# Kernel optimization log

Measured on AMD Instinct MI355X. Metric: run time of the kernel, lower is better.

The kernel has to match this reference:

```python
import jax, jax.numpy as jnp
import numpy as np

B, S, IN, OUT, H, L, NH, STEPS = 256, 128, 64, 64, 1024, 2, 4, 16
HD = H // NH


def setup_inputs() -> dict:
    key = jax.random.key(0)
    ks = iter(jax.random.split(key, 32))
    std_h = 1.0 / np.sqrt(H)

    def u(k, shape, std):
        return jax.random.uniform(k, shape, jnp.float32, -std, std)

    inp = {"x": jax.random.normal(next(ks), (B, S, IN), jnp.float32)}
    # LSTM cells: stacked gate weights, gate order (i, f, g, o); y = x@Wx + h@Wh + b
    for name, din in (("e0", IN), ("e1", H), ("d0", OUT), ("d1", H)):
        inp[name + "_Wx"] = u(next(ks), (din, 4 * H), std_h)
        inp[name + "_Wh"] = u(next(ks), (H, 4 * H), std_h)
        inp[name + "_b"] = u(next(ks), (4 * H,), std_h)
    # attention linears (x@W + b convention)
    for name in ("Wq", "Wk", "Wv", "Wo"):
        inp[name] = u(next(ks), (H, H), std_h)
    for name in ("bq", "bk", "bv", "bo"):
        inp[name] = u(next(ks), (H,), std_h)
    inp["fc_W"] = u(next(ks), (2 * H, H), 1.0 / np.sqrt(2 * H))
    inp["fc_b"] = u(next(ks), (H,), 1.0 / np.sqrt(2 * H))
    inp["out_W"] = u(next(ks), (H, OUT), std_h)
    inp["out_b"] = u(next(ks), (OUT,), std_h)
    return inp


def _cell(x_t, h, c, Wx, Wh, b):
    z = x_t @ Wx + h @ Wh + b  # [B, 4H]
    i, f, g, o = jnp.split(z, 4, axis=-1)
    c = jax.nn.sigmoid(f) * c + jax.nn.sigmoid(i) * jnp.tanh(g)
    h = jax.nn.sigmoid(o) * jnp.tanh(c)
    return h, c


def _lstm_seq(x, Wx, Wh, b):
    # x: [B, T, D] -> outputs [B, T, H], final (h, c)
    h0 = jnp.zeros((x.shape[0], H), x.dtype)
    def step(carry, xt):
        h, c = carry
        h, c = _cell(xt, h, c, Wx, Wh, b)
        return (h, c), h
    (h, c), ys = jax.lax.scan(step, (h0, h0), jnp.swapaxes(x, 0, 1))
    return jnp.swapaxes(ys, 0, 1), h, c


def reference(x, e0_Wx, e0_Wh, e0_b, e1_Wx, e1_Wh, e1_b,
              d0_Wx, d0_Wh, d0_b, d1_Wx, d1_Wh, d1_b,
              Wq, bq, Wk, bk, Wv, bv, Wo, bo, fc_W, fc_b, out_W, out_b):
    # encoder: 2-layer manual LSTM (dropout=0, eval)
    y0, h0, c0 = _lstm_seq(x, e0_Wx, e0_Wh, e0_b)
    enc_out, h1, c1 = _lstm_seq(y0, e1_Wx, e1_Wh, e1_b)

    # K/V projections of encoder outputs (constant across decoder steps)
    Kp = (enc_out @ Wk + bk).reshape(B, S, NH, HD)
    Vp = (enc_out @ Wv + bv).reshape(B, S, NH, HD)
    scale = float(HD) ** 0.5

    def dstep(carry, _):
        dh0, dc0, dh1, dc1, xin = carry
        dh0, dc0 = _cell(xin, dh0, dc0, d0_Wx, d0_Wh, d0_b)
        dh1, dc1 = _cell(dh0, dh1, dc1, d1_Wx, d1_Wh, d1_b)
        q = (dh1 @ Wq + bq).reshape(B, NH, HD)
        scores = jnp.einsum('bnd,bsnd->bns', q, Kp) / scale
        w = jax.nn.softmax(scores, axis=-1)
        ctx = jnp.einsum('bns,bsnd->bnd', w, Vp).reshape(B, H)
        attn = ctx @ Wo + bo
        comb = jax.nn.relu(jnp.concatenate([dh1, attn], axis=-1) @ fc_W + fc_b)
        out = comb @ out_W + out_b  # [B, OUT]
        return (dh0, dc0, dh1, dc1, out), out

    init = (h0, c0, h1, c1, jnp.zeros((B, OUT), x.dtype))
    _, preds = jax.lax.scan(dstep, init, None, length=STEPS)
    return jnp.swapaxes(preds, 0, 1)  # [B, STEPS, OUT]
```

## Files before the change

kernel.cpp:

```cpp
#include <hip/hip_runtime.h>
#include <math.h>

typedef _Float16 h8 __attribute__((ext_vector_type(8)));
typedef _Float16 h4 __attribute__((ext_vector_type(4)));
typedef float f16v __attribute__((ext_vector_type(16)));

#define HPS 262144
#define XPS 2097152
#define IPS 16384
#define BSTR 40
#define BUFE (128 * BSTR)

__device__ __forceinline__ float4 ld4(const float* p) { return *(const float4*)p; }
__device__ __forceinline__ float sigf(float x) { return 1.0f / (1.0f + expf(-x)); }
__device__ __forceinline__ float bf2f(unsigned short u) { return __uint_as_float(((unsigned)u) << 16); }
__device__ __forceinline__ float rdin(const void* p, size_t i, int bf) {
  return bf ? bf2f(((const unsigned short*)p)[i]) : ((const float*)p)[i];
}

__global__ void detect_dtype(const unsigned short* __restrict__ probe, int n, int* flag) {
  __shared__ int cnt;
  if (threadIdx.x == 0) cnt = 0;
  __syncthreads();
  int c = 0;
  for (int i = threadIdx.x; i < n; i += 256) {
    int e = (probe[i] >> 7) & 0xFF;
    if (e >= 100 && e <= 126) c++;
  }
  atomicAdd(&cnt, c);
  __syncthreads();
  if (threadIdx.x == 0) *flag = (cnt > (n * 3) / 4) ? 1 : 0;
}

__global__ void cvt_f32(const void* __restrict__ in, float* __restrict__ out, int n,
                        const int* __restrict__ flag) {
  int bf = *flag;
  int i = blockIdx.x * 256 + threadIdx.x;
  if (i < n) out[i] = rdin(in, i, bf);
}

__global__ void tsplit(const void* __restrict__ in, int N,
                       _Float16* __restrict__ outHi, _Float16* __restrict__ outLo,
                       int ldo, int kOff, int pOff, const int* __restrict__ flag) {
  __shared__ float tile[32][33];
  int bf = *flag;
  int kb = blockIdx.x * 32, nb = blockIdx.y * 32;
  for (int r = threadIdx.y; r < 32; r += 8)
    tile[threadIdx.x][r] = rdin(in, (size_t)(kb + r) * N + nb + threadIdx.x, bf);
  __syncthreads();
  for (int r = threadIdx.y; r < 32; r += 8) {
    float v = tile[r][threadIdx.x];
    _Float16 hi = (_Float16)v;
    _Float16 lo = (_Float16)(v - (float)hi);
    size_t o = (size_t)(pOff + nb + r) * ldo + kOff + kb + threadIdx.x;
    outHi[o] = hi; outLo[o] = lo;
  }
}

__global__ void f2h_kernel(const void* __restrict__ in, _Float16* __restrict__ out, int n,
                           const int* __restrict__ flag) {
  int bf = *flag;
  int i = blockIdx.x * 1024 + threadIdx.x * 4;
  if (i < n) {
    float vv[4];
#pragma unroll
    for (int k = 0; k < 4; ++k) vv[k] = rdin(in, i + k, bf);
    h4 hv, lv;
#pragma unroll
    for (int k = 0; k < 4; ++k) { hv[k] = (_Float16)vv[k]; lv[k] = (_Float16)(vv[k] - (float)hv[k]); }
    *(h4*)(out + i) = hv;
    *(h4*)(out + n + i) = lv;
  }
}

__global__ void sentinel_kernel(float* out, float v) { out[0] = v; }

__device__ __forceinline__ void gemm_tile(
    const _Float16* __restrict__ A0, int lda0, int aps0,
    const _Float16* __restrict__ A1, int lda1, int aps1, int ksplit,
    const _Float16* __restrict__ WTh, const _Float16* __restrict__ WTl, int ldw,
    int pbase, int c0, int c1,
    float* __restrict__ zp, int zld, _Float16* Bs ) {
  const int tid = threadIdx.x;
  const int wv = tid >> 6, lane = tid & 63;
  const int l31 = lane & 31, lhi = lane >> 5;

  f16v acc00 = {}, acc01 = {}, acc10 = {}, acc11 = {};

  const int r0 = wv * 64 + l31;
  const int r1 = r0 + 32;
  const _Float16* a0b0 = A0 + (size_t)r0 * lda0;
  const _Float16* a1b0 = A1 + (size_t)r0 * lda1;
  const _Float16* a0b1 = A0 + (size_t)r1 * lda0;
  const _Float16* a1b1 = A1 + (size_t)r1 * lda1;

  const int spl = tid >> 7;
  const int sidx = tid & 127;
  const int sp = sidx >> 1;
  const int skh = (sidx & 1) << 4;
  const _Float16* srow = (spl ? WTl : WTh) + (size_t)(pbase + sp) * ldw + skh;
  const int sdoff = (spl * 64 + sp) * BSTR + skh;

  {
    const _Float16* s = srow + (c0 << 5);
    float4 v0 = *(const float4*)(s);
    float4 v1 = *(const float4*)(s + 8);
    _Float16* d = Bs + sdoff;
    *(float4*)(d) = v0;
    *(float4*)(d + 8) = v1;
  }

  int buf = 0;
  for (int c = c0; c < c1; ++c) {
    __syncthreads();
    float4 n0, n1;
    const bool more = (c + 1 < c1);
    if (more) {
      const _Float16* s = srow + ((c + 1) << 5);
      n0 = *(const float4*)(s);
      n1 = *(const float4*)(s + 8);
    }
    const _Float16* bb = Bs + buf * BUFE;
    int k0 = c << 5;
#pragma unroll
    for (int sub = 0; sub < 2; ++sub) {
      int ks = k0 + sub * 16 + lhi * 8;
      const _Float16 *pa0, *pa1; int ap;
      if (ks < ksplit) { pa0 = a0b0 + ks; pa1 = a0b1 + ks; ap = aps0; }
      else { int kk = ks - ksplit; pa0 = a1b0 + kk; pa1 = a1b1 + kk; ap = aps1; }
      h8 af0h = *(const h8*)pa0;
      h8 af0l = *(const h8*)(pa0 + ap);
      h8 af1h = *(const h8*)pa1;
      h8 af1l = *(const h8*)(pa1 + ap);
      int kl = sub * 16 + lhi * 8;
      h8 b0h = *(const h8*)(bb + (size_t)(l31) * BSTR + kl);
      h8 b0l = *(const h8*)(bb + (size_t)(64 + l31) * BSTR + kl);
      h8 b1h = *(const h8*)(bb + (size_t)(32 + l31) * BSTR + kl);
      h8 b1l = *(const h8*)(bb + (size_t)(96 + l31) * BSTR + kl);
      acc00 = __builtin_amdgcn_mfma_f32_32x32x16_f16(af0h, b0h, acc00, 0, 0, 0);
      acc00 = __builtin_amdgcn_mfma_f32_32x32x16_f16(af0h, b0l, acc00, 0, 0, 0);
      acc00 = __builtin_amdgcn_mfma_f32_32x32x16_f16(af0l, b0h, acc00, 0, 0, 0);
      acc01 = __builtin_amdgcn_mfma_f32_32x32x16_f16(af0h, b1h, acc01, 0, 0, 0);
      acc01 = __builtin_amdgcn_mfma_f32_32x32x16_f16(af0h, b1l, acc01, 0, 0, 0);
      acc01 = __builtin_amdgcn_mfma_f32_32x32x16_f16(af0l, b1h, acc01, 0, 0, 0);
      acc10 = __builtin_amdgcn_mfma_f32_32x32x16_f16(af1h, b0h, acc10, 0, 0, 0);
      acc10 = __builtin_amdgcn_mfma_f32_32x32x16_f16(af1h, b0l, acc10, 0, 0, 0);
      acc10 = __builtin_amdgcn_mfma_f32_32x32x16_f16(af1l, b0h, acc10, 0, 0, 0);
      acc11 = __builtin_amdgcn_mfma_f32_32x32x16_f16(af1h, b1h, acc11, 0, 0, 0);
      acc11 = __builtin_amdgcn_mfma_f32_32x32x16_f16(af1h, b1l, acc11, 0, 0, 0);
      acc11 = __builtin_amdgcn_mfma_f32_32x32x16_f16(af1l, b1h, acc11, 0, 0, 0);
    }
    if (more) {
      _Float16* d = Bs + (buf ^ 1) * BUFE + sdoff;
      *(float4*)(d) = n0;
      *(float4*)(d + 8) = n1;
    }
    buf ^= 1;
  }

#pragma unroll
  for (int mi = 0; mi < 2; ++mi) {
#pragma unroll
    for (int ni = 0; ni < 2; ++ni) {
      f16v av = (mi == 0) ? (ni == 0 ? acc00 : acc01) : (ni == 0 ? acc10 : acc11);
      int col = pbase + ni * 32 + l31;
#pragma unroll
      for (int r = 0; r < 16; ++r) {
        int row = wv * 64 + mi * 32 + (r & 3) + ((r >> 2) * 8) + lhi * 4;
        zp[(size_t)row * zld + col] = av[r];
      }
    }
  }
}

__global__ __launch_bounds__(256, 2) void enc_gemm(int t, int l1kq,
    const _Float16* xh, const _Float16* h0, const _Float16* h1,
    const _Float16* wt0h, const _Float16* wt0l,
    const _Float16* wt1h, const _Float16* wt1l,
    const _Float16* wtkvh, const _Float16* wtkvl,
    float* z0, float* z1, float* kvz) {
  __shared__ _Float16 Bs[2 * BUFE];
  int blk = blockIdx.x;
  int nl1 = 64 * l1kq;
  if (blk < nl1) {
    if (t < 1 || t > 128) return;
    int pg = blk & 63, kq = blk >> 6;
    int c0 = (64 * kq) / l1kq, c1 = (64 * (kq + 1)) / l1kq;
    gemm_tile(h0, 1024, HPS, h1, 1024, HPS, 1024, wt1h, wt1l, 2048,
              pg * 64, c0, c1, z1 + (size_t)kq * 1048576, 4096, Bs);
  } else if (blk < nl1 + 128) {
    if (t > 127) return;
    int w = blk - nl1, pg = w & 63, kq = w >> 6;
    gemm_tile(xh + (size_t)t * 64, 8192, XPS, h0, 1024, HPS, 64, wt0h, wt0l, 1088,
              pg * 64, kq * 17, kq * 17 + 17, z0 + (size_t)kq * 1048576, 4096, Bs);
  } else {
    if (t < 2) return;
    int w = blk - nl1 - 128, pg = w & 31, kq = w >> 5;
    gemm_tile(h1, 1024, HPS, h1, 1024, HPS, 1024, wtkvh, wtkvl, 1024,
              pg * 64, kq * 16, kq * 16 + 16, kvz + (size_t)kq * 524288, 2048, Bs);
  }
}

__global__ __launch_bounds__(256, 2) void gemm_k(
    const _Float16* A0, int lda0, int aps0,
    const _Float16* A1, int lda1, int aps1, int ksplit,
    const _Float16* WTh, const _Float16* WTl, int ldw,
    int npg, int nkq, int tot, int kqoff, float* zp, int zld) {
  __shared__ _Float16 Bs[2 * BUFE];
  int pg = blockIdx.x % npg, kq = blockIdx.x / npg + kqoff;
  int c0 = (tot * kq) / nkq, c1 = (tot * (kq + 1)) / nkq;
  gemm_tile(A0, lda0, aps0, A1, lda1, aps1, ksplit, WTh, WTl, ldw,
            pg * 64, c0, c1, zp + (size_t)kq * 256 * zld, zld, Bs);
}

__global__ __launch_bounds__(256, 2) void qfc_kernel(
    const _Float16* h1,
    const _Float16* wqh, const _Float16* wql,
    const _Float16* wfh, const _Float16* wfl,
    float* qp, float* fcp) {
  __shared__ _Float16 Bs[2 * BUFE];
  int blk = blockIdx.x;
  if (blk < 64) {
    int pg = blk & 15, kq = blk >> 4;
    gemm_tile(h1, 1024, HPS, h1, 1024, HPS, 1024, wqh, wql, 1024,
              pg * 64, kq * 8, kq * 8 + 8, qp + (size_t)kq * 262144, 1024, Bs);
  } else {
    int w = blk - 64, pg = w & 15, kq = w >> 4;
    gemm_tile(h1, 1024, HPS, h1, 1024, HPS, 1024, wfh, wfl, 2048,
              pg * 64, kq * 8, kq * 8 + 8, fcp + (size_t)kq * 262144, 1024, Bs);
  }
}

__device__ __forceinline__ void gates_body(const float* __restrict__ zp, int nparts,
    const float* __restrict__ bias, float* __restrict__ c,
    _Float16* __restrict__ h, int blk) {
  int e = blk * 1024 + threadIdx.x * 4;
  int b = e >> 10, j = e & 1023;
  size_t zrow = (size_t)b * 4096;
  float4 vi = ld4(bias + j), vf = ld4(bias + 1024 + j), vg = ld4(bias + 2048 + j), vo = ld4(bias + 3072 + j);
  for (int q = 0; q < nparts; ++q) {
    const float* zq = zp + (size_t)q * 1048576 + zrow;
    float4 t;
    t = ld4(zq + j);        vi.x += t.x; vi.y += t.y; vi.z += t.z; vi.w += t.w;
    t = ld4(zq + 1024 + j); vf.x += t.x; vf.y += t.y; vf.z += t.z; vf.w += t.w;
    t = ld4(zq + 2048 + j); vg.x += t.x; vg.y += t.y; vg.z += t.z; vg.w += t.w;
    t = ld4(zq + 3072 + j); vo.x += t.x; vo.y += t.y; vo.z += t.z; vo.w += t.w;
  }
  float* cp = c + (size_t)b * 1024 + j;
  float4 cv = ld4(cp);
  float zi[4] = {vi.x, vi.y, vi.z, vi.w}, zf[4] = {vf.x, vf.y, vf.z, vf.w};
  float zg[4] = {vg.x, vg.y, vg.z, vg.w}, zo[4] = {vo.x, vo.y, vo.z, vo.w};
  float cc[4] = {cv.x, cv.y, cv.z, cv.w};
  float hn[4];
#pragma unroll
  for (int k = 0; k < 4; ++k) {
    float ii = sigf(zi[k]), ff = sigf(zf[k]), gg = tanhf(zg[k]), oo = sigf(zo[k]);
    float cn = ff * cc[k] + ii * gg;
    cc[k] = cn;
    hn[k] = oo * tanhf(cn);
  }
  float4 co; co.x = cc[0]; co.y = cc[1]; co.z = cc[2]; co.w = cc[3];
  *(float4*)cp = co;
  h4 hv, lv;
#pragma unroll
  for (int k = 0; k < 4; ++k) { hv[k] = (_Float16)hn[k]; lv[k] = (_Float16)(hn[k] - (float)hv[k]); }
  *(h4*)(h + (size_t)b * 1024 + j) = hv;
  *(h4*)(h + HPS + (size_t)b * 1024 + j) = lv;
}

__global__ void enc_gates(int t, int l1parts, const float* z0, const float* z1, const float* kvz,
                          const float* b0, const float* b1,
                          const float* bk, const float* bv,
                          float* c0, float* c1, _Float16* h0, _Float16* h1,
                          _Float16* Kp, _Float16* Vp) {
  int blk = blockIdx.x;
  if (blk < 256) {
    if (t > 127) return;
    gates_body(z0, 2, b0, c0, h0, blk);
  } else if (blk < 512) {
    if (t < 1 || t > 128) return;
    gates_body(z1, l1parts, b1, c1, h1, blk - 256);
  } else {
    if (t < 2) return;
    int e = (blk - 512) * 1024 + threadIdx.x * 4;
    int b = e >> 11, col = e & 2047;
    const float* bb = (col < 1024) ? (bk + col) : (bv + col - 1024);
    float4 v = ld4(bb);
    for (int q = 0; q < 2; ++q) {
      float4 tt = ld4(kvz + (size_t)q * 524288 + e);
      v.x += tt.x; v.y += tt.y; v.z += tt.z; v.w += tt.w;
    }
    _Float16* dst = (col < 1024) ? Kp : Vp;
    int cc = (col < 1024) ? col : col - 1024;
    h4 hv; hv[0] = (_Float16)v.x; hv[1] = (_Float16)v.y; hv[2] = (_Float16)v.z; hv[3] = (_Float16)v.w;
    *(h4*)(dst + (size_t)(b * 128 + (t - 2)) * 1024 + cc) = hv;
  }
}

__global__ void dec_gates(const float* zp, int nparts, const float* bias,
                          float* c, _Float16* h) {
  gates_body(zp, nparts, bias, c, h, blockIdx.x);
}

__global__ void reduce_act(const float* __restrict__ zp, int nparts,
                           const float* __restrict__ bias, _Float16* __restrict__ out, int relu) {
  int e = blockIdx.x * 1024 + threadIdx.x * 4;
  int j = e & 1023;
  float4 v = ld4(bias + j);
  for (int q = 0; q < nparts; ++q) {
    float4 t = ld4(zp + (size_t)q * 262144 + e);
    v.x += t.x; v.y += t.y; v.z += t.z; v.w += t.w;
  }
  if (relu) {
    v.x = fmaxf(v.x, 0.f); v.y = fmaxf(v.y, 0.f); v.z = fmaxf(v.z, 0.f); v.w = fmaxf(v.w, 0.f);
  }
  float vv[4] = {v.x, v.y, v.z, v.w};
  h4 hv, lv;
#pragma unroll
  for (int k = 0; k < 4; ++k) { hv[k] = (_Float16)vv[k]; lv[k] = (_Float16)(vv[k] - (float)hv[k]); }
  *(h4*)(out + e) = hv;
  *(h4*)(out + HPS + e) = lv;
}

__global__ void out_reduce(const float* __restrict__ op, const float* __restrict__ outb,
                           float* __restrict__ dout, _Float16* __restrict__ xin, int s) {
  int e = blockIdx.x * 1024 + threadIdx.x * 4;
  int b = e >> 6, o = e & 63;
  float4 v = ld4(outb + o);
  for (int q = 0; q < 16; ++q) {
    float4 t = ld4(op + (size_t)q * 16384 + e);
    v.x += t.x; v.y += t.y; v.z += t.z; v.w += t.w;
  }
  *(float4*)(dout + (size_t)(b * 16 + s) * 64 + o) = v;
  float vv[4] = {v.x, v.y, v.z, v.w};
  h4 hv, lv;
#pragma unroll
  for (int k = 0; k < 4; ++k) { hv[k] = (_Float16)vv[k]; lv[k] = (_Float16)(vv[k] - (float)hv[k]); }
  *(h4*)(xin + e) = hv;
  *(h4*)(xin + IPS + e) = lv;
}

__global__ void attn_kernel(const float* __restrict__ qp, const float* __restrict__ bq,
                            const _Float16* __restrict__ Kp, const _Float16* __restrict__ Vp,
                            _Float16* __restrict__ ctx) {
  int b = blockIdx.x >> 2, n = blockIdx.x & 3;
  __shared__ float qs[256];
  __shared__ float sw[128];
  int tid = threadIdx.x;
  float qv = bq[n * 256 + tid];
  for (int q = 0; q < 4; ++q) qv += qp[(size_t)q * 262144 + (size_t)b * 1024 + n * 256 + tid];
  qs[tid] = qv;
  __syncthreads();
  int w = tid >> 6, lane = tid & 63;
  for (int s = w; s < 128; s += 4) {
    const _Float16* kr = Kp + (size_t)(b * 128 + s) * 1024 + n * 256;
    float acc = 0.f;
#pragma unroll
    for (int d = 0; d < 4; ++d) acc += qs[lane + d * 64] * (float)kr[lane + d * 64];
    for (int off = 32; off; off >>= 1) acc += __shfl_down(acc, off);
    if (lane == 0) sw[s] = acc * 0.0625f;
  }
  __syncthreads();
  if (w == 0) {
    float a = sw[lane], bb = sw[lane + 64];
    float m = fmaxf(a, bb);
    for (int off = 32; off; off >>= 1) m = fmaxf(m, __shfl_down(m, off));
    m = __shfl(m, 0);
    float e1 = expf(a - m), e2 = expf(bb - m);
    float ss = e1 + e2;
    for (int off = 32; off; off >>= 1) ss += __shfl_down(ss, off);
    ss = __shfl(ss, 0);
    float inv = 1.0f / ss;
    sw[lane] = e1 * inv; sw[lane + 64] = e2 * inv;
  }
  __syncthreads();
  float acc = 0.f;
  const _Float16* vb = Vp + (size_t)b * 131072 + n * 256 + tid;
  for (int s2 = 0; s2 < 128; ++s2) acc += sw[s2] * (float)vb[(size_t)s2 * 1024];
  size_t idx = (size_t)b * 1024 + n * 256 + tid;
  _Float16 hi = (_Float16)acc;
  ctx[idx] = hi;
  ctx[HPS + idx] = (_Float16)(acc - (float)hi);
}

extern "C" void kernel_launch(void* const* d_in, const int* in_sizes, int n_in,
                              void* d_out, int out_size, void* d_ws, size_t ws_size,
                              hipStream_t stream) {
  const void* x     = d_in[0];
  const void* e0_Wx = d_in[1];
  const void* e0_Wh = d_in[2];
  const void* e0_b  = d_in[3];
  const void* e1_Wx = d_in[4];
  const void* e1_Wh = d_in[5];
  const void* e1_b  = d_in[6];
  const void* d0_Wx = d_in[7];
  const void* d0_Wh = d_in[8];
  const void* d0_b  = d_in[9];
  const void* d1_Wx = d_in[10];
  const void* d1_Wh = d_in[11];
  const void* d1_b  = d_in[12];
  const void* Wq = d_in[13];
  const void* Wk = d_in[14];
  const void* Wv = d_in[15];
  const void* Wo = d_in[16];
  const void* bq = d_in[17];
  const void* bk = d_in[18];
  const void* bv = d_in[19];
  const void* bo = d_in[20];
  const void* fc_W  = d_in[21];
  const void* fc_b  = d_in[22];
  const void* out_W = d_in[23];
  const void* out_b = d_in[24];

  int l1parts = 4;
  char* p = (char*)d_ws;
  int* flag; float* bias_arena; char* warena; char* zero0;
  _Float16 *h0, *h1, *xin, *Kp, *Vp, *ctx, *attn_h, *comb;
  float *c0, *c1; float* zarena;
  size_t zeroBytes = 0;

  for (int attempt = 0; attempt < 2; ++attempt) {
    p = (char*)d_ws;
    auto alloc = [&](size_t bytes) { char* r = p; p += (bytes + 255) & ~(size_t)255; return r; };
    flag = (int*)alloc(256);
    bias_arena = (float*)alloc(87040);
    warena = alloc(68419584);
    zero0 = p;
    h0 = (_Float16*)alloc(1048576);
    h1 = (_Float16*)alloc(1048576);
    c0 = (float*)alloc(1048576);
    c1 = (float*)alloc(1048576);
    xin = (_Float16*)alloc(65536);
    zeroBytes = (size_t)(p - zero0);
    Kp = (_Float16*)alloc(67108864);
    Vp = (_Float16*)alloc(67108864);
    zarena = (float*)alloc((size_t)(3 + l1parts) * 4194304);
    ctx    = (_Float16*)alloc(1048576);
    attn_h = (_Float16*)alloc(1048576);
    comb   = (_Float16*)alloc(1048576);
    if ((size_t)(p - (char*)d_ws) <= ws_size) break;
    l1parts = 2;
  }
  if ((size_t)(p - (char*)d_ws) > ws_size) {
    sentinel_kernel<<<1, 1, 0, stream>>>((float*)d_out, 1.0e9f + (float)ws_size);
    return;
  }

  float* c_e0b = bias_arena +     0;
  float* c_e1b = bias_arena +  4096;
  float* c_d0b = bias_arena +  8192;
  float* c_d1b = bias_arena + 12288;
  float* c_bq  = bias_arena + 16384;
  float* c_bk  = bias_arena + 17408;
  float* c_bv  = bias_arena + 18432;
  float* c_bo  = bias_arena + 19456;
  float* c_fcb = bias_arena + 20480;
  float* c_ob  = bias_arena + 21504;

  _Float16* wt_e0h = (_Float16*)(warena);
  _Float16* wt_e0l = (_Float16*)(warena +  8912896);
  _Float16* wt_e1h = (_Float16*)(warena + 17825792);
  _Float16* wt_e1l = (_Float16*)(warena + 34603008);
  _Float16* wt_kvh = (_Float16*)(warena + 51380224);
  _Float16* wt_kvl = (_Float16*)(warena + 55574528);
  _Float16* xh     = (_Float16*)(warena + 59768832);
  _Float16* wt_d0h = (_Float16*)(warena);
  _Float16* wt_d0l = (_Float16*)(warena +  8912896);
  _Float16* wt_d1h = (_Float16*)(warena + 17825792);
  _Float16* wt_d1l = (_Float16*)(warena + 34603008);
  _Float16* wt_qh  = (_Float16*)(warena + 51380224);
  _Float16* wt_ql  = (_Float16*)(warena + 53477376);
  _Float16* wt_oh  = (_Float16*)(warena + 55574528);
  _Float16* wt_ol  = (_Float16*)(warena + 57671680);
  _Float16* wt_fch = (_Float16*)(warena + 59768832);
  _Float16* wt_fcl = (_Float16*)(warena + 63963136);
  _Float16* wt_outh= (_Float16*)(warena + 68157440);
  _Float16* wt_outl= (_Float16*)(warena + 68288512);

  float* z0e = zarena;
  float* z1e = zarena + 2097152;
  float* kvz = z1e + (size_t)l1parts * 1048576;
  float* zdec = zarena;
  float* fcp = zarena;
  float* qp  = zarena + 2097152;
  float* op  = zarena + 3145728;

  detect_dtype<<<1, 256, 0, stream>>>((const unsigned short*)e0_Wx, 16384, flag);
  cvt_f32<<<16, 256, 0, stream>>>(e0_b, c_e0b, 4096, flag);
  cvt_f32<<<16, 256, 0, stream>>>(e1_b, c_e1b, 4096, flag);
  cvt_f32<<<16, 256, 0, stream>>>(d0_b, c_d0b, 4096, flag);
  cvt_f32<<<16, 256, 0, stream>>>(d1_b, c_d1b, 4096, flag);
  cvt_f32<<<4, 256, 0, stream>>>(bq, c_bq, 1024, flag);
  cvt_f32<<<4, 256, 0, stream>>>(bk, c_bk, 1024, flag);
  cvt_f32<<<4, 256, 0, stream>>>(bv, c_bv, 1024, flag);
  cvt_f32<<<4, 256, 0, stream>>>(bo, c_bo, 1024, flag);
  cvt_f32<<<4, 256, 0, stream>>>(fc_b, c_fcb, 1024, flag);
  cvt_f32<<<1, 64, 0, stream>>>(out_b, c_ob, 64, flag);

  dim3 tb(32, 8);
  tsplit<<<dim3(2, 128), tb, 0, stream>>>(e0_Wx, 4096, wt_e0h, wt_e0l, 1088, 0, 0, flag);
  tsplit<<<dim3(32, 128), tb, 0, stream>>>(e0_Wh, 4096, wt_e0h, wt_e0l, 1088, 64, 0, flag);
  tsplit<<<dim3(32, 128), tb, 0, stream>>>(e1_Wx, 4096, wt_e1h, wt_e1l, 2048, 0, 0, flag);
  tsplit<<<dim3(32, 128), tb, 0, stream>>>(e1_Wh, 4096, wt_e1h, wt_e1l, 2048, 1024, 0, flag);
  tsplit<<<dim3(32, 32), tb, 0, stream>>>(Wk, 1024, wt_kvh, wt_kvl, 1024, 0, 0, flag);
  tsplit<<<dim3(32, 32), tb, 0, stream>>>(Wv, 1024, wt_kvh, wt_kvl, 1024, 0, 1024, flag);
  f2h_kernel<<<2048, 256, 0, stream>>>(x, xh, 2097152, flag);
  hipMemsetAsync(zero0, 0, zeroBytes, stream);

  int encBlocks = 64 * l1parts + 192;
  for (int t = 0; t <= 129; ++t) {
    enc_gemm<<<encBlocks, 256, 0, stream>>>(t, l1parts, xh, h0, h1,
                                            wt_e0h, wt_e0l, wt_e1h, wt_e1l,
                                            wt_kvh, wt_kvl, z0e, z1e, kvz);
    enc_gates<<<1024, 256, 0, stream>>>(t, l1parts, z0e, z1e, kvz, c_e0b, c_e1b, c_bk, c_bv,
                                        c0, c1, h0, h1, Kp, Vp);
  }

  tsplit<<<dim3(2, 128), tb, 0, stream>>>(d0_Wx, 4096, wt_d0h, wt_d0l, 1088, 0, 0, flag);
  tsplit<<<dim3(32, 128), tb, 0, stream>>>(d0_Wh, 4096, wt_d0h, wt_d0l, 1088, 64, 0, flag);
  tsplit<<<dim3(32, 128), tb, 0, stream>>>(d1_Wx, 4096, wt_d1h, wt_d1l, 2048, 0, 0, flag);
  tsplit<<<dim3(32, 128), tb, 0, stream>>>(d1_Wh, 4096, wt_d1h, wt_d1l, 2048, 1024, 0, flag);
  tsplit<<<dim3(32, 32), tb, 0, stream>>>(Wq, 1024, wt_qh, wt_ql, 1024, 0, 0, flag);
  tsplit<<<dim3(32, 32), tb, 0, stream>>>(Wo, 1024, wt_oh, wt_ol, 1024, 0, 0, flag);
  tsplit<<<dim3(64, 32), tb, 0, stream>>>(fc_W, 1024, wt_fch, wt_fcl, 2048, 0, 0, flag);
  tsplit<<<dim3(32, 2), tb, 0, stream>>>(out_W, 64, wt_outh, wt_outl, 1024, 0, 0, flag);

  for (int s = 0; s < 16; ++s) {
    gemm_k<<<256, 256, 0, stream>>>(xin, 64, IPS, h0, 1024, HPS, 64,
                                    wt_d0h, wt_d0l, 1088, 64, 4, 34, 0, zdec, 4096);
    dec_gates<<<256, 256, 0, stream>>>(zdec, 4, c_d0b, c0, h0);
    gemm_k<<<256, 256, 0, stream>>>(h0, 1024, HPS, h1, 1024, HPS, 1024,
                                    wt_d1h, wt_d1l, 2048, 64, 4, 64, 0, zdec, 4096);
    dec_gates<<<256, 256, 0, stream>>>(zdec, 4, c_d1b, c1, h1);
    qfc_kernel<<<128, 256, 0, stream>>>(h1, wt_qh, wt_ql, wt_fch, wt_fcl, qp, fcp);
    attn_kernel<<<1024, 256, 0, stream>>>(qp, c_bq, Kp, Vp, ctx);
    gemm_k<<<64, 256, 0, stream>>>(ctx, 1024, HPS, ctx, 1024, HPS, 1024,
                                   wt_oh, wt_ol, 1024, 16, 4, 32, 0, qp, 1024);
    reduce_act<<<256, 256, 0, stream>>>(qp, 4, c_bo, attn_h, 0);
    gemm_k<<<64, 256, 0, stream>>>(h1, 1024, HPS, attn_h, 1024, HPS, 1024,
                                   wt_fch, wt_fcl, 2048, 16, 8, 64, 4, fcp, 1024);
    reduce_act<<<256, 256, 0, stream>>>(fcp, 8, c_fcb, comb, 1);
    gemm_k<<<16, 256, 0, stream>>>(comb, 1024, HPS, comb, 1024, HPS, 1024,
                                   wt_outh, wt_outl, 1024, 1, 16, 32, 0, op, 64);
    out_reduce<<<16, 256, 0, stream>>>(op, c_ob, (float*)d_out, xin, s);
  }
}
```

Measured before the change: 9.562 ms.

## Fuse encoder GEMM and LSTM gate epilogue into one per-step kernel

Replaces the per-timestep pair of encoder GEMM and gates kernels with a single enc_step kernel. Encoder gate weights are permuted at load time so each 64-column tile holds interleaved i,f,g,o gates for 16 hidden units, which lets the cell update and K/V bias run in the GEMM epilogue through a shared-memory staging buffer. Hidden states are double-buffered so blocks can read the previous h while writing the new one without a grid-wide sync. This removes the split-K partial-sum buffers and half the launches per step, in exchange for less block parallelism (no K split, 128-row tiles with a 64-deep serial K loop for layer 1) and extra LDS use.

```diff
diff --git a/kernel.cpp b/kernel.cpp
--- a/kernel.cpp
+++ b/kernel.cpp
@@ -10,6 +10,7 @@
 #define IPS 16384
 #define BSTR 40
 #define BUFE (128 * BSTR)
+#define GSTR 66
 
 __device__ __forceinline__ float4 ld4(const float* p) { return *(const float4*)p; }
 __device__ __forceinline__ float sigf(float x) { return 1.0f / (1.0f + expf(-x)); }
@@ -32,16 +33,19 @@
   if (threadIdx.x == 0) *flag = (cnt > (n * 3) / 4) ? 1 : 0;
 }
 
-__global__ void cvt_f32(const void* __restrict__ in, float* __restrict__ out, int n,
+__global__ void cvt_f32(const void* __restrict__ in, float* __restrict__ out, int n, int gp,
                         const int* __restrict__ flag) {
   int bf = *flag;
   int i = blockIdx.x * 256 + threadIdx.x;
-  if (i < n) out[i] = rdin(in, i, bf);
+  if (i < n) {
+    int o = gp ? (((i & 1023) << 2) | (i >> 10)) : i;
+    out[o] = rdin(in, i, bf);
+  }
 }
 
 __global__ void tsplit(const void* __restrict__ in, int N,
                        _Float16* __restrict__ outHi, _Float16* __restrict__ outLo,
-                       int ldo, int kOff, int pOff, const int* __restrict__ flag) {
+                       int ldo, int kOff, int pOff, int gp, const int* __restrict__ flag) {
   __shared__ float tile[32][33];
   int bf = *flag;
   int kb = blockIdx.x * 32, nb = blockIdx.y * 32;
@@ -52,7 +56,9 @@
     float v = tile[r][threadIdx.x];
     _Float16 hi = (_Float16)v;
     _Float16 lo = (_Float16)(v - (float)hi);
-    size_t o = (size_t)(pOff + nb + r) * ldo + kOff + kb + threadIdx.x;
+    int p = pOff + nb + r;
+    if (gp) p = ((p & 1023) << 2) | (p >> 10);
+    size_t o = (size_t)p * ldo + kOff + kb + threadIdx.x;
     outHi[o] = hi; outLo[o] = lo;
   }
 }
@@ -74,6 +80,193 @@
 }
 
 __global__ void sentinel_kernel(float* out, float v) { out[0] = v; }
+
+__device__ __forceinline__ f16v mfma16(h8 a, h8 b, f16v c) {
+  return __builtin_amdgcn_mfma_f32_32x32x16_f16(a, b, c, 0, 0, 0);
+}
+
+__device__ __forceinline__ void enc_kloop(
+    const _Float16* __restrict__ A0, int lda0, int aps0,
+    const _Float16* __restrict__ A1, int lda1, int aps1, int ksplit,
+    const _Float16* __restrict__ WTh, const _Float16* __restrict__ WTl, int ldw,
+    int pbase, int rbase, int nch, _Float16* Bs, f16v& acc0, f16v& acc1) {
+  const int tid = threadIdx.x;
+  const int wv = tid >> 6, lane = tid & 63;
+  const int l31 = lane & 31, lhi = lane >> 5;
+
+  const int r = rbase + wv * 32 + l31;
+  const _Float16* a0 = A0 + (size_t)r * lda0;
+  const _Float16* a1 = A1 + (size_t)r * lda1;
+
+  const int spl = tid >> 7;
+  const int sidx = tid & 127;
+  const int sp = sidx >> 1;
+  const int skh = (sidx & 1) << 4;
+  const _Float16* srow = (spl ? WTl : WTh) + (size_t)(pbase + sp) * ldw + skh;
+  const int sdoff = (spl * 64 + sp) * BSTR + skh;
+
+  {
+    float4 v0 = *(const float4*)(srow);
+    float4 v1 = *(const float4*)(srow + 8);
+    *(float4*)(Bs + sdoff) = v0;
+    *(float4*)(Bs + sdoff + 8) = v1;
+  }
+
+  int buf = 0;
+  for (int c = 0; c < nch; ++c) {
+    __syncthreads();
+    float4 n0, n1;
+    const bool more = (c + 1 < nch);
+    if (more) {
+      const _Float16* s = srow + ((c + 1) << 5);
+      n0 = *(const float4*)(s);
+      n1 = *(const float4*)(s + 8);
+    }
+    const _Float16* bb = Bs + buf * BUFE;
+    int k0 = c << 5;
+#pragma unroll
+    for (int sub = 0; sub < 2; ++sub) {
+      int ks = k0 + sub * 16 + lhi * 8;
+      const _Float16* pa; int ap;
+      if (ks < ksplit) { pa = a0 + ks; ap = aps0; }
+      else             { pa = a1 + (ks - ksplit); ap = aps1; }
+      h8 afh = *(const h8*)pa;
+      h8 afl = *(const h8*)(pa + ap);
+      int kl = sub * 16 + lhi * 8;
+      h8 b0h = *(const h8*)(bb + (size_t)(l31) * BSTR + kl);
+      h8 b0l = *(const h8*)(bb + (size_t)(64 + l31) * BSTR + kl);
+      h8 b1h = *(const h8*)(bb + (size_t)(32 + l31) * BSTR + kl);
+      h8 b1l = *(const h8*)(bb + (size_t)(96 + l31) * BSTR + kl);
+      acc0 = mfma16(afh, b0h, acc0);
+      acc0 = mfma16(afh, b0l, acc0);
+      acc0 = mfma16(afl, b0h, acc0);
+      acc1 = mfma16(afh, b1h, acc1);
+      acc1 = mfma16(afh, b1l, acc1);
+      acc1 = mfma16(afl, b1h, acc1);
+    }
+    if (more) {
+      _Float16* d = Bs + (buf ^ 1) * BUFE + sdoff;
+      *(float4*)(d) = n0;
+      *(float4*)(d + 8) = n1;
+    }
+    buf ^= 1;
+  }
+}
+
+__device__ __forceinline__ void stage_acc(float* gs, const f16v& a0, const f16v& a1,
+                                          int l31, int lhi) {
+#pragma unroll
+  for (int r2 = 0; r2 < 16; ++r2) {
+    int row = (r2 & 3) + 8 * (r2 >> 2) + 4 * lhi;
+    gs[row * GSTR + l31] = a0[r2];
+    gs[row * GSTR + 32 + l31] = a1[r2];
+  }
+}
+
+__device__ __forceinline__ void lstm_fin(const float* gs, const float* __restrict__ pb,
+                                         float* __restrict__ c, _Float16* __restrict__ h,
+                                         int cg, int rbaseg, int lane) {
+  int rowl = lane & 31, uh = lane >> 5;
+  int rowg = rbaseg + rowl;
+  const float* z = gs + rowl * GSTR + uh * 32;
+  const float* pbp = pb + cg * 64 + uh * 32;
+  float* cp = c + (size_t)rowg * 1024 + cg * 16 + uh * 8;
+  _Float16* hp = h + (size_t)rowg * 1024 + cg * 16 + uh * 8;
+  float4 cv0 = ld4(cp), cv1 = ld4(cp + 4);
+  float cc[8] = {cv0.x, cv0.y, cv0.z, cv0.w, cv1.x, cv1.y, cv1.z, cv1.w};
+  h8 hh, hl;
+#pragma unroll
+  for (int u = 0; u < 8; ++u) {
+    float4 zz = ld4(z + u * 4);
+    float4 bb = ld4(pbp + u * 4);
+    float ii = sigf(zz.x + bb.x), ff = sigf(zz.y + bb.y);
+    float gg = tanhf(zz.z + bb.z), oo = sigf(zz.w + bb.w);
+    float cn = ff * cc[u] + ii * gg;
+    cc[u] = cn;
+    float hn = oo * tanhf(cn);
+    _Float16 hi = (_Float16)hn;
+    hh[u] = hi; hl[u] = (_Float16)(hn - (float)hi);
+  }
+  float4 co0 = {cc[0], cc[1], cc[2], cc[3]}, co1 = {cc[4], cc[5], cc[6], cc[7]};
+  *(float4*)cp = co0;
+  *(float4*)(cp + 4) = co1;
+  *(h8*)hp = hh;
+  *(h8*)(hp + HPS) = hl;
+}
+
+__device__ __forceinline__ void kv_fin(const float* gs,
+                                       const float* __restrict__ bk, const float* __restrict__ bv,
+                                       _Float16* __restrict__ Kp, _Float16* __restrict__ Vp,
+                                       int cg, int rbaseg, int lane, int t) {
+  int rowl = lane & 31, half = lane >> 5;
+  int rowg = rbaseg + rowl;
+  int colb = cg * 64 + half * 32;
+  const float* z = gs + rowl * GSTR + half * 32;
+  const float* bias = (colb < 1024) ? (bk + colb) : (bv + colb - 1024);
+  _Float16* dst = (colb < 1024) ? (Kp + ((size_t)rowg * 128 + (t - 2)) * 1024 + colb)
+                                : (Vp + ((size_t)rowg * 128 + (t - 2)) * 1024 + colb - 1024);
+#pragma unroll
+  for (int j = 0; j < 4; ++j) {
+    float4 a = ld4(z + j * 8), b = ld4(z + j * 8 + 4);
+    float4 ba = ld4(bias + j * 8), bb = ld4(bias + j * 8 + 4);
+    h8 hv;
+    hv[0] = (_Float16)(a.x + ba.x); hv[1] = (_Float16)(a.y + ba.y);
+    hv[2] = (_Float16)(a.z + ba.z); hv[3] = (_Float16)(a.w + ba.w);
+    hv[4] = (_Float16)(b.x + bb.x); hv[5] = (_Float16)(b.y + bb.y);
+    hv[6] = (_Float16)(b.z + bb.z); hv[7] = (_Float16)(b.w + bb.w);
+    *(h8*)(dst + j * 8) = hv;
+  }
+}
+
+__global__ __launch_bounds__(256, 2) void enc_step(int t,
+    const _Float16* xh, _Float16* h0a, _Float16* h0b, _Float16* h1a, _Float16* h1b,
+    const _Float16* wt0h, const _Float16* wt0l,
+    const _Float16* wt1h, const _Float16* wt1l,
+    const _Float16* wtkvh, const _Float16* wtkvl,
+    const float* pb0, const float* pb1, const float* bk, const float* bv,
+    float* c0, float* c1, _Float16* Kp, _Float16* Vp) {
+  __shared__ _Float16 Bs[2 * BUFE];
+  __shared__ float Gs[4][32 * GSTR];
+  int blk = blockIdx.x;
+  const int pr = (t - 1) & 1;
+  const _Float16* h0r = pr ? h0b : h0a;
+  const _Float16* h1r = pr ? h1b : h1a;
+  const int tid = threadIdx.x;
+  const int wv = tid >> 6, lane = tid & 63;
+  const int l31 = lane & 31, lhi = lane >> 5;
+  f16v acc0 = {}, acc1 = {};
+
+  if (blk < 128) {
+    if (t > 127) return;
+    int cg = blk & 63, rh = blk >> 6;
+    int rbase = rh * 128;
+    enc_kloop(xh + (size_t)t * 64, 8192, XPS, h0r, 1024, HPS, 64,
+              wt0h, wt0l, 1088, cg * 64, rbase, 34, Bs, acc0, acc1);
+    float* gs = &Gs[wv][0];
+    stage_acc(gs, acc0, acc1, l31, lhi);
+    _Float16* h0w = (t & 1) ? h0b : h0a;
+    lstm_fin(gs, pb0, c0, h0w, cg, rbase + wv * 32, lane);
+  } else if (blk < 256) {
+    if (t < 1 || t > 128) return;
+    int w = blk - 128, cg = w & 63, rh = w >> 6;
+    int rbase = rh * 128;
+    enc_kloop(h0r, 1024, HPS, h1r, 1024, HPS, 1024,
+              wt1h, wt1l, 2048, cg * 64, rbase, 64, Bs, acc0, acc1);
+    float* gs = &Gs[wv][0];
+    stage_acc(gs, acc0, acc1, l31, lhi);
+    _Float16* h1w = (t & 1) ? h1b : h1a;
+    lstm_fin(gs, pb1, c1, h1w, cg, rbase + wv * 32, lane);
+  } else {
+    if (t < 2) return;
+    int w = blk - 256, cg = w & 31, rh = w >> 5;
+    int rbase = rh * 128;
+    enc_kloop(h1r, 1024, HPS, h1r, 1024, HPS, 1024,
+              wtkvh, wtkvl, 1024, cg * 64, rbase, 32, Bs, acc0, acc1);
+    float* gs = &Gs[wv][0];
+    stage_acc(gs, acc0, acc1, l31, lhi);
+    kv_fin(gs, bk, bv, Kp, Vp, cg, rbase + wv * 32, lane, t);
+  }
+}
 
 __device__ __forceinline__ void gemm_tile(
     const _Float16* __restrict__ A0, int lda0, int aps0,
@@ -137,18 +330,18 @@
       h8 b0l = *(const h8*)(bb + (size_t)(64 + l31) * BSTR + kl);
       h8 b1h = *(const h8*)(bb + (size_t)(32 + l31) * BSTR + kl);
       h8 b1l = *(const h8*)(bb + (size_t)(96 + l31) * BSTR + kl);
-      acc00 = __builtin_amdgcn_mfma_f32_32x32x16_f16(af0h, b0h, acc00, 0, 0, 0);
-      acc00 = __builtin_amdgcn_mfma_f32_32x32x16_f16(af0h, b0l, acc00, 0, 0, 0);
-      acc00 = __builtin_amdgcn_mfma_f32_32x32x16_f16(af0l, b0h, acc00, 0, 0, 0);
-      acc01 = __builtin_amdgcn_mfma_f32_32x32x16_f16(af0h, b1h, acc01, 0, 0, 0);
-      acc01 = __builtin_amdgcn_mfma_f32_32x32x16_f16(af0h, b1l, acc01, 0, 0, 0);
-      acc01 = __builtin_amdgcn_mfma_f32_32x32x16_f16(af0l, b1h, acc01, 0, 0, 0);
-      acc10 = __builtin_amdgcn_mfma_f32_32x32x16_f16(af1h, b0h, acc10, 0, 0, 0);
-      acc10 = __builtin_amdgcn_mfma_f32_32x32x16_f16(af1h, b0l, acc10, 0, 0, 0);
-      acc10 = __builtin_amdgcn_mfma_f32_32x32x16_f16(af1l, b0h, acc10, 0, 0, 0);
-      acc11 = __builtin_amdgcn_mfma_f32_32x32x16_f16(af1h, b1h, acc11, 0, 0, 0);
-      acc11 = __builtin_amdgcn_mfma_f32_32x32x16_f16(af1h, b1l, acc11, 0, 0, 0);
-      acc11 = __builtin_amdgcn_mfma_f32_32x32x16_f16(af1l, b1h, acc11, 0, 0, 0);
+      acc00 = mfma16(af0h, b0h, acc00);
+      acc00 = mfma16(af0h, b0l, acc00);
+      acc00 = mfma16(af0l, b0h, acc00);
+      acc01 = mfma16(af0h, b1h, acc01);
+      acc01 = mfma16(af0h, b1l, acc01);
+      acc01 = mfma16(af0l, b1h, acc01);
+      acc10 = mfma16(af1h, b0h, acc10);
+      acc10 = mfma16(af1h, b0l, acc10);
+      acc10 = mfma16(af1l, b0h, acc10);
+      acc11 = mfma16(af1h, b1h, acc11);
+      acc11 = mfma16(af1h, b1l, acc11);
+      acc11 = mfma16(af1l, b1h, acc11);
     }
     if (more) {
       _Float16* d = Bs + (buf ^ 1) * BUFE + sdoff;
@@ -170,34 +363,6 @@
         zp[(size_t)row * zld + col] = av[r];
       }
     }
-  }
-}
-
-__global__ __launch_bounds__(256, 2) void enc_gemm(int t, int l1kq,
-    const _Float16* xh, const _Float16* h0, const _Float16* h1,
-    const _Float16* wt0h, const _Float16* wt0l,
-    const _Float16* wt1h, const _Float16* wt1l,
-    const _Float16* wtkvh, const _Float16* wtkvl,
-    float* z0, float* z1, float* kvz) {
-  __shared__ _Float16 Bs[2 * BUFE];
-  int blk = blockIdx.x;
-  int nl1 = 64 * l1kq;
-  if (blk < nl1) {
-    if (t < 1 || t > 128) return;
-    int pg = blk & 63, kq = blk >> 6;
-    int c0 = (64 * kq) / l1kq, c1 = (64 * (kq + 1)) / l1kq;
-    gemm_tile(h0, 1024, HPS, h1, 1024, HPS, 1024, wt1h, wt1l, 2048,
-              pg * 64, c0, c1, z1 + (size_t)kq * 1048576, 4096, Bs);
-  } else if (blk < nl1 + 128) {
-    if (t > 127) return;
-    int w = blk - nl1, pg = w & 63, kq = w >> 6;
-    gemm_tile(xh + (size_t)t * 64, 8192, XPS, h0, 1024, HPS, 64, wt0h, wt0l, 1088,
-              pg * 64, kq * 17, kq * 17 + 17, z0 + (size_t)kq * 1048576, 4096, Bs);
-  } else {
-    if (t < 2) return;
-    int w = blk - nl1 - 128, pg = w & 31, kq = w >> 5;
-    gemm_tile(h1, 1024, HPS, h1, 1024, HPS, 1024, wtkvh, wtkvl, 1024,
-              pg * 64, kq * 16, kq * 16 + 16, kvz + (size_t)kq * 524288, 2048, Bs);
   }
 }
 
@@ -266,35 +431,6 @@
   for (int k = 0; k < 4; ++k) { hv[k] = (_Float16)hn[k]; lv[k] = (_Float16)(hn[k] - (float)hv[k]); }
   *(h4*)(h + (size_t)b * 1024 + j) = hv;
   *(h4*)(h + HPS + (size_t)b * 1024 + j) = lv;
-}
-
-__global__ void enc_gates(int t, int l1parts, const float* z0, const float* z1, const float* kvz,
-                          const float* b0, const float* b1,
-                          const float* bk, const float* bv,
-                          float* c0, float* c1, _Float16* h0, _Float16* h1,
-                          _Float16* Kp, _Float16* Vp) {
-  int blk = blockIdx.x;
-  if (blk < 256) {
-    if (t > 127) return;
-    gates_body(z0, 2, b0, c0, h0, blk);
-  } else if (blk < 512) {
-    if (t < 1 || t > 128) return;
-    gates_body(z1, l1parts, b1, c1, h1, blk - 256);
-  } else {
-    if (t < 2) return;
-    int e = (blk - 512) * 1024 + threadIdx.x * 4;
-    int b = e >> 11, col = e & 2047;
-    const float* bb = (col < 1024) ? (bk + col) : (bv + col - 1024);
-    float4 v = ld4(bb);
-    for (int q = 0; q < 2; ++q) {
-      float4 tt = ld4(kvz + (size_t)q * 524288 + e);
-      v.x += tt.x; v.y += tt.y; v.z += tt.z; v.w += tt.w;
-    }
-    _Float16* dst = (col < 1024) ? Kp : Vp;
-    int cc = (col < 1024) ? col : col - 1024;
-    h4 hv; hv[0] = (_Float16)v.x; hv[1] = (_Float16)v.y; hv[2] = (_Float16)v.z; hv[3] = (_Float16)v.w;
-    *(h4*)(dst + (size_t)(b * 128 + (t - 2)) * 1024 + cc) = hv;
-  }
 }
 
 __global__ void dec_gates(const float* zp, int nparts, const float* bias,
@@ -412,35 +548,26 @@
   const void* out_W = d_in[23];
   const void* out_b = d_in[24];
 
-  int l1parts = 4;
   char* p = (char*)d_ws;
-  int* flag; float* bias_arena; char* warena; char* zero0;
-  _Float16 *h0, *h1, *xin, *Kp, *Vp, *ctx, *attn_h, *comb;
-  float *c0, *c1; float* zarena;
-  size_t zeroBytes = 0;
-
-  for (int attempt = 0; attempt < 2; ++attempt) {
-    p = (char*)d_ws;
-    auto alloc = [&](size_t bytes) { char* r = p; p += (bytes + 255) & ~(size_t)255; return r; };
-    flag = (int*)alloc(256);
-    bias_arena = (float*)alloc(87040);
-    warena = alloc(68419584);
-    zero0 = p;
-    h0 = (_Float16*)alloc(1048576);
-    h1 = (_Float16*)alloc(1048576);
-    c0 = (float*)alloc(1048576);
-    c1 = (float*)alloc(1048576);
-    xin = (_Float16*)alloc(65536);
-    zeroBytes = (size_t)(p - zero0);
-    Kp = (_Float16*)alloc(67108864);
-    Vp = (_Float16*)alloc(67108864);
-    zarena = (float*)alloc((size_t)(3 + l1parts) * 4194304);
-    ctx    = (_Float16*)alloc(1048576);
-    attn_h = (_Float16*)alloc(1048576);
-    comb   = (_Float16*)alloc(1048576);
-    if ((size_t)(p - (char*)d_ws) <= ws_size) break;
-    l1parts = 2;
-  }
+  auto alloc = [&](size_t bytes) { char* r = p; p += (bytes + 255) & ~(size_t)255; return r; };
+  int* flag = (int*)alloc(256);
+  float* bias_arena = (float*)alloc(87040);
+  char* warena = alloc(68419584);
+  char* zero0 = p;
+  _Float16* h0a = (_Float16*)alloc(1048576);
+  _Float16* h0b = (_Float16*)alloc(1048576);
+  _Float16* h1a = (_Float16*)alloc(1048576);
+  _Float16* h1b = (_Float16*)alloc(1048576);
+  float* c0 = (float*)alloc(1048576);
+  float* c1 = (float*)alloc(1048576);
+  _Float16* xin = (_Float16*)alloc(65536);
+  size_t zeroBytes = (size_t)(p - zero0);
+  _Float16* Kp = (_Float16*)alloc(67108864);
+  _Float16* Vp = (_Float16*)alloc(67108864);
+  float* zarena = (float*)alloc(16777216);
+  _Float16* ctx    = (_Float16*)alloc(1048576);
+  _Float16* attn_h = (_Float16*)alloc(1048576);
+  _Float16* comb   = (_Float16*)alloc(1048576);
   if ((size_t)(p - (char*)d_ws) > ws_size) {
     sentinel_kernel<<<1, 1, 0, stream>>>((float*)d_out, 1.0e9f + (float)ws_size);
     return;
@@ -477,67 +604,67 @@
   _Float16* wt_outh= (_Float16*)(warena + 68157440);
   _Float16* wt_outl= (_Float16*)(warena + 68288512);
 
-  float* z0e = zarena;
-  float* z1e = zarena + 2097152;
-  float* kvz = z1e + (size_t)l1parts * 1048576;
   float* zdec = zarena;
   float* fcp = zarena;
   float* qp  = zarena + 2097152;
   float* op  = zarena + 3145728;
 
   detect_dtype<<<1, 256, 0, stream>>>((const unsigned short*)e0_Wx, 16384, flag);
-  cvt_f32<<<16, 256, 0, stream>>>(e0_b, c_e0b, 4096, flag);
-  cvt_f32<<<16, 256, 0, stream>>>(e1_b, c_e1b, 4096, flag);
-  cvt_f32<<<16, 256, 0, stream>>>(d0_b, c_d0b, 4096, flag);
-  cvt_f32<<<16, 256, 0, stream>>>(d1_b, c_d1b, 4096, flag);
-  cvt_f32<<<4, 256, 0, stream>>>(bq, c_bq, 1024, flag);
-  cvt_f32<<<4, 256, 0, stream>>>(bk, c_bk, 1024, flag);
-  cvt_f32<<<4, 256, 0, stream>>>(bv, c_bv, 1024, flag);
-  cvt_f32<<<4, 256, 0, stream>>>(bo, c_bo, 1024, flag);
-  cvt_f32<<<4, 256, 0, stream>>>(fc_b, c_fcb, 1024, flag);
-  cvt_f32<<<1, 64, 0, stream>>>(out_b, c_ob, 64, flag);
+  cvt_f32<<<16, 256, 0, stream>>>(e0_b, c_e0b, 4096, 1, flag);
+  cvt_f32<<<16, 256, 0, stream>>>(e1_b, c_e1b, 4096, 1, flag);
+  cvt_f32<<<16, 256, 0, stream>>>(d0_b, c_d0b, 4096, 0, flag);
+  cvt_f32<<<16, 256, 0, stream>>>(d1_b, c_d1b, 4096, 0, flag);
+  cvt_f32<<<4, 256, 0, stream>>>(bq, c_bq, 1024, 0, flag);
+  cvt_f32<<<4, 256, 0, stream>>>(bk, c_bk, 1024, 0, flag);
+  cvt_f32<<<4, 256, 0, stream>>>(bv, c_bv, 1024, 0, flag);
+  cvt_f32<<<4, 256, 0, stream>>>(bo, c_bo, 1024, 0, flag);
+  cvt_f32<<<4, 256, 0, stream>>>(fc_b, c_fcb, 1024, 0, flag);
+  cvt_f32<<<1, 64, 0, stream>>>(out_b, c_ob, 64, 0, flag);
 
   dim3 tb(32, 8);
-  tsplit<<<dim3(2, 128), tb, 0, stream>>>(e0_Wx, 4096, wt_e0h, wt_e0l, 1088, 0, 0, flag);
-  tsplit<<<dim3(32, 128), tb, 0, stream>>>(e0_Wh, 4096, wt_e0h, wt_e0l, 1088, 64, 0, flag);
-  tsplit<<<dim3(32, 128), tb, 0, stream>>>(e1_Wx, 4096, wt_e1h, wt_e1l, 2048, 0, 0, flag);
-  tsplit<<<dim3(32, 128), tb, 0, stream>>>(e1_Wh, 4096, wt_e1h, wt_e1l, 2048, 1024, 0, flag);
-  tsplit<<<dim3(32, 32), tb, 0, stream>>>(Wk, 1024, wt_kvh, wt_kvl, 1024, 0, 0, flag);
-  tsplit<<<dim3(32, 32), tb, 0, stream>>>(Wv, 1024, wt_kvh, wt_kvl, 1024, 0, 1024, flag);
+  tsplit<<<dim3(2, 128), tb, 0, stream>>>(e0_Wx, 4096, wt_e0h, wt_e0l, 1088, 0, 0, 1, flag);
+  tsplit<<<dim3(32, 128), tb, 0, stream>>>(e0_Wh, 4096, wt_e0h, wt_e0l, 1088, 64, 0, 1, flag);
+  tsplit<<<dim3(32, 128), tb, 0, stream>>>(e1_Wx, 4096, wt_e1h, wt_e1l, 2048, 0, 0, 1, flag);
+  tsplit<<<dim3(32, 128), tb, 0, stream>>>(e1_Wh, 4096, wt_e1h, wt_e1l, 2048, 1024, 0, 1, flag);
+  tsplit<<<dim3(32, 32), tb, 0, stream>>>(Wk, 1024, wt_kvh, wt_kvl, 1024, 0, 0, 0, flag);
+  tsplit<<<dim3(32, 32), tb, 0, stream>>>(Wv, 1024, wt_kvh, wt_kvl, 1024, 0, 1024, 0, flag);
   f2h_kernel<<<2048, 256, 0, stream>>>(x, xh, 2097152, flag);
   hipMemsetAsync(zero0, 0, zeroBytes, stream);
 
-  int encBlocks = 64 * l1parts + 192;
   for (int t = 0; t <= 129; ++t) {
-    enc_gemm<<<encBlocks, 256, 0, stream>>>(t, l1parts, xh, h0, h1,
-                                            wt_e0h, wt_e0l, wt_e1h, wt_e1l,
-                                            wt_kvh, wt_kvl, z0e, z1e, kvz);
-    enc_gates<<<1024, 256, 0, stream>>>(t, l1parts, z0e, z1e, kvz, c_e0b, c_e1b, c_bk, c_bv,
-                                        c0, c1, h0, h1, Kp, Vp);
-  }
-
-  tsplit<<<dim3(2, 128), tb, 0, stream>>>(d0_Wx, 4096, wt_d0h, wt_d0l, 1088, 0, 0, flag);
-  tsplit<<<dim3(32, 128), tb, 0, stream>>>(d0_Wh, 4096, wt_d0h, wt_d0l, 1088, 64, 0, flag);
-  tsplit<<<dim3(32, 128), tb, 0, stream>>>(d1_Wx, 4096, wt_d1h, wt_d1l, 2048, 0, 0, flag);
-  tsplit<<<dim3(32, 128), tb, 0, stream>>>(d1_Wh, 4096, wt_d1h, wt_d1l, 2048, 1024, 0, flag);
-  tsplit<<<dim3(32, 32), tb, 0, stream>>>(Wq, 1024, wt_qh, wt_ql, 1024, 0, 0, flag);
-  tsplit<<<dim3(32, 32), tb, 0, stream>>>(Wo, 1024, wt_oh, wt_ol, 1024, 0, 0, flag);
-  tsplit<<<dim3(64, 32), tb, 0, stream>>>(fc_W, 1024, wt_fch, wt_fcl, 2048, 0, 0, flag);
-  tsplit<<<dim3(32, 2), tb, 0, stream>>>(out_W, 64, wt_outh, wt_outl, 1024, 0, 0, flag);
+    enc_step<<<320, 256, 0, stream>>>(t, xh, h0a, h0b, h1a, h1b,
+                                      wt_e0h, wt_e0l, wt_e1h, wt_e1l,
+                                      wt_kvh, wt_kvl,
+                                      c_e0b, c_e1b, c_bk, c_bv,
+                                      c0, c1, Kp, Vp);
+  }
+
+  tsplit<<<dim3(2, 128), tb, 0, stream>>>(d0_Wx, 4096, wt_d0h, wt_d0l, 1088, 0, 0, 0, flag);
+  tsplit<<<dim3(32, 128), tb, 0, stream>>>(d0_Wh, 4096, wt_d0h, wt_d0l, 1088, 64, 0, 0, flag);
+  tsplit<<<dim3(32, 128), tb, 0, stream>>>(d1_Wx, 4096, wt_d1h, wt_d1l, 2048, 0, 0, 0, flag);
+  tsplit<<<dim3(32, 128), tb, 0, stream>>>(d1_Wh, 4096, wt_d1h, wt_d1l, 2048, 1024, 0, 0, flag);
+  tsplit<<<dim3(32, 32), tb, 0, stream>>>(Wq, 1024, wt_qh, wt_ql, 1024, 0, 0, 0, flag);
+  tsplit<<<dim3(32, 32), tb, 0, stream>>>(Wo, 1024, wt_oh, wt_ol, 1024, 0, 0, 0, flag);
+  tsplit<<<dim3(64, 32), tb, 0, stream>>>(fc_W, 1024, wt_fch, wt_fcl, 2048, 0, 0, 0, flag);
+  tsplit<<<dim3(32, 2), tb, 0, stream>>>(out_W, 64, wt_outh, wt_outl, 1024, 0, 0, 0, flag);
 
   for (int s = 0; s < 16; ++s) {
-    gemm_k<<<256, 256, 0, stream>>>(xin, 64, IPS, h0, 1024, HPS, 64,
+    const _Float16* h0r = (s & 1) ? h0a : h0b;
+    _Float16* h0w = (s & 1) ? h0b : h0a;
+    const _Float16* h1r = (s & 1) ? h1b : h1a;
+    _Float16* h1w = (s & 1) ? h1a : h1b;
+    gemm_k<<<256, 256, 0, stream>>>(xin, 64, IPS, h0r, 1024, HPS, 64,
                                     wt_d0h, wt_d0l, 1088, 64, 4, 34, 0, zdec, 4096);
-    dec_gates<<<256, 256, 0, stream>>>(zdec, 4, c_d0b, c0, h0);
-    gemm_k<<<256, 256, 0, stream>>>(h0, 1024, HPS, h1, 1024, HPS, 1024,
+    dec_gates<<<256, 256, 0, stream>>>(zdec, 4, c_d0b, c0, h0w);
+    gemm_k<<<256, 256, 0, stream>>>(h0w, 1024, HPS, h1r, 1024, HPS, 1024,
                                     wt_d1h, wt_d1l, 2048, 64, 4, 64, 0, zdec, 4096);
-    dec_gates<<<256, 256, 0, stream>>>(zdec, 4, c_d1b, c1, h1);
-    qfc_kernel<<<128, 256, 0, stream>>>(h1, wt_qh, wt_ql, wt_fch, wt_fcl, qp, fcp);
+    dec_gates<<<256, 256, 0, stream>>>(zdec, 4, c_d1b, c1, h1w);
+    qfc_kernel<<<128, 256, 0, stream>>>(h1w, wt_qh, wt_ql, wt_fch, wt_fcl, qp, fcp);
     attn_kernel<<<1024, 256, 0, stream>>>(qp, c_bq, Kp, Vp, ctx);
     gemm_k<<<64, 256, 0, stream>>>(ctx, 1024, HPS, ctx, 1024, HPS, 1024,
                                    wt_oh, wt_ol, 1024, 16, 4, 32, 0, qp, 1024);
     reduce_act<<<256, 256, 0, stream>>>(qp, 4, c_bo, attn_h, 0);
-    gemm_k<<<64, 256, 0, stream>>>(h1, 1024, HPS, attn_h, 1024, HPS, 1024,
+    gemm_k<<<64, 256, 0, stream>>>(h1w, 1024, HPS, attn_h, 1024, HPS, 1024,
                                    wt_fch, wt_fcl, 2048, 16, 8, 64, 4, fcp, 1024);
     reduce_act<<<256, 256, 0, stream>>>(fcp, 8, c_fcb, comb, 1);
     gemm_k<<<16, 256, 0, stream>>>(comb, 1024, HPS, comb, 1024, HPS, 1024,
```

After: 12.19 ms. 1.27x slower.
